# Performance work log

Measured on AMD Instinct MI355X. Metric: run time of the kernel, lower is better.

## Reference

```python
import jax, jax.numpy as jnp
import numpy as np

N = 100_000      # num nodes
R = 7            # num relations
D = 64           # input_dim == output_dim
E = 1_600_000    # num edges
EDIM = 16        # edge_input_dim


def setup_inputs() -> dict:
    key = jax.random.key(0)
    ks = jax.random.split(key, 10)
    node_in = jax.random.randint(ks[0], (E,), 0, N)
    node_out = jax.random.randint(ks[1], (E,), 0, N)
    relation = jax.random.randint(ks[2], (E,), 0, R)
    edge_list = jnp.stack([node_in, node_out, relation], axis=1)  # (E, 3)
    x = jax.random.normal(ks[3], (N, D), dtype=jnp.float32)
    edge_weight = jax.random.uniform(ks[4], (E,), dtype=jnp.float32)
    edge_feature = jax.random.normal(ks[5], (E, EDIM), dtype=jnp.float32)
    s = 1.0 / np.sqrt(R * D)
    W_lin = jax.random.uniform(ks[6], (D, R * D), minval=-s, maxval=s, dtype=jnp.float32)
    b_lin = jnp.zeros((D,), jnp.float32)
    s2 = 1.0 / np.sqrt(D)
    W_self = jax.random.uniform(ks[7], (D, D), minval=-s2, maxval=s2, dtype=jnp.float32)
    b_self = jnp.zeros((D,), jnp.float32)
    s3 = 1.0 / np.sqrt(EDIM)
    W_edge = jax.random.uniform(ks[8], (D, EDIM), minval=-s3, maxval=s3, dtype=jnp.float32)
    b_edge = jnp.zeros((D,), jnp.float32)
    return {"x": x, "edge_list": edge_list, "edge_weight": edge_weight,
            "edge_feature": edge_feature, "W_lin": W_lin, "b_lin": b_lin,
            "W_self": W_self, "b_self": b_self, "W_edge": W_edge, "b_edge": b_edge}


def reference(x, edge_list, edge_weight, edge_feature, W_lin, b_lin, W_self, b_self, W_edge, b_edge):
    node_in, node_out, relation = edge_list[:, 0], edge_list[:, 1], edge_list[:, 2]
    # destination index in the flattened (node, relation) space
    seg = node_out * R + relation  # (E,)
    # sparse.mm(adj.T, x): scatter w * x[src] into (N*R, D)
    msg = edge_weight[:, None] * x[node_in]  # (E, D)
    update = jax.ops.segment_sum(msg, seg, num_segments=N * R)  # (N*R, D)
    # edge feature branch: edge_linear then weighted scatter_add
    edge_msg = (edge_feature @ W_edge.T + b_edge) * edge_weight[:, None]  # (E, D)
    update = update + jax.ops.segment_sum(edge_msg, seg, num_segments=N * R)
    update = update.reshape(N, R * D)
    out = update @ W_lin.T + b_lin + x @ W_self.T + b_self
    return jax.nn.relu(out)
```

## Files before the change

kernel.cpp:

```cpp
#include <hip/hip_runtime.h>
#include <hip/hip_bf16.h>
#include <hip/hip_fp16.h>

#define N_NODES 100000
#define R_REL   7
#define E_EDGES 1600000
#define EDIM    16
#define KTOT    640
#define AROWB   1280
#define CAP     56
#define CSTR    16
#define CHUNK   16


#define ASWZ(row, cb) ((row) * AROWB + ((cb) ^ (((row) & 7) << 4)))

typedef __bf16 bf16_t;
typedef bf16_t bf16x8 __attribute__((ext_vector_type(8)));
typedef float  f32x4  __attribute__((ext_vector_type(4)));
typedef unsigned long long u64;

#define RFL(v) __builtin_amdgcn_readfirstlane(v)
#define RL(v, l) __builtin_amdgcn_readlane(v, l)


__global__ __launch_bounds__(256) void k_pre(
    const float* __restrict__ x, const int* __restrict__ el,
    const float* __restrict__ wgt,
    const float* __restrict__ W_lin, const float* __restrict__ W_self,
    const float* __restrict__ W_edge, const float* __restrict__ b_edge,
    int* __restrict__ cnt, bf16_t* __restrict__ xb, bf16_t* __restrict__ Bp,
    u64* __restrict__ recs8)
{
    const int t = blockIdx.x * 256 + threadIdx.x;

    if (t < (N_NODES * 64) / 16) {
        const float4* xp = (const float4*)(x + (size_t)t * 16);
        float4 v0 = xp[0], v1 = xp[1], v2 = xp[2], v3 = xp[3];
        bf16x8 o0 = {(bf16_t)v0.x, (bf16_t)v0.y, (bf16_t)v0.z, (bf16_t)v0.w,
                     (bf16_t)v1.x, (bf16_t)v1.y, (bf16_t)v1.z, (bf16_t)v1.w};
        bf16x8 o1 = {(bf16_t)v2.x, (bf16_t)v2.y, (bf16_t)v2.z, (bf16_t)v2.w,
                     (bf16_t)v3.x, (bf16_t)v3.y, (bf16_t)v3.z, (bf16_t)v3.w};
        *(bf16x8*)(xb + (size_t)t * 16)     = o0;
        *(bf16x8*)(xb + (size_t)t * 16 + 8) = o1;
    }

    if (t < KTOT * 64) {
        int k = t >> 6;
        int j = t & 63;
        float v;
        if (k < 448) {
            v = W_lin[j * 448 + k];
        } else if (k < 512) {
            v = W_self[j * 64 + (k - 448)];
        } else if (k < 624) {
            int r = (k - 512) >> 4, kk = (k - 512) & 15;
            float sacc = 0.f;
            for (int d = 0; d < 64; d++)
                sacc = fmaf(W_lin[j * 448 + r * 64 + d], W_edge[d * 16 + kk], sacc);
            v = sacc;
        } else if (k < 631) {
            int r = k - 624;
            float sacc = 0.f;
            for (int d = 0; d < 64; d++)
                sacc = fmaf(W_lin[j * 448 + r * 64 + d], b_edge[d], sacc);
            v = sacc;
        } else {
            v = 0.f;
        }
        Bp[((k >> 3) * 64 + j) * 8 + (k & 7)] = (bf16_t)v;
    }

    if (t < E_EDGES / 4) {
        const int4* ep = (const int4*)(el + (size_t)t * 12);
        int4 q0 = ep[0], q1 = ep[1], q2 = ep[2];
        float4 w4 = *(const float4*)(wgt + (size_t)t * 4);
        const int e = t * 4;
        const int srcs[4] = {q0.x, q0.w, q1.z, q2.y};
        const int dsts[4] = {q0.y, q1.x, q1.w, q2.z};
        const int rels[4] = {q0.z, q1.y, q2.x, q2.w};
        const float ws[4] = {w4.x, w4.y, w4.z, w4.w};
        int slot[4];
#pragma unroll
        for (int i = 0; i < 4; i++)
            slot[i] = atomicAdd(&cnt[dsts[i] * CSTR], 1);
#pragma unroll
        for (int i = 0; i < 4; i++) {
            unsigned u0 = (unsigned)srcs[i] | ((unsigned)rels[i] << 17)
                        | ((unsigned)((e + i) & 0xFFF) << 20);
            unsigned u1 = ((unsigned)(e + i) >> 12)
                        | (__float_as_uint(ws[i]) & 0xFFFFFE00u);
            if (slot[i] < CAP)
                recs8[(size_t)slot[i] * N_NODES + dsts[i]] = ((u64)u1 << 32) | u0;
        }
    }
}


__global__ __launch_bounds__(256, 6) void k_main(
    const bf16_t* __restrict__ xb, const float* __restrict__ ef,
    const float* __restrict__ b_lin, const float* __restrict__ b_self,
    const int* __restrict__ cnt, const u64* __restrict__ recs8,
    const bf16_t* __restrict__ Bp, float* __restrict__ out)
{
    __shared__ __align__(16) unsigned char A[16 * AROWB];
    const int wave = threadIdx.x >> 6;
    const int lane = threadIdx.x & 63;
    const int lef  = lane & 15;
    const int nodeBase = blockIdx.x * 16;
    const int n0 = nodeBase + wave * 4;

    int md[4];
    u64 rw[4];
#pragma unroll
    for (int i = 0; i < 4; i++) {
        const int row = wave * 4 + i;
        md[i] = RFL(min(cnt[(n0 + i) * CSTR], CAP));
        rw[i] = (lane < md[i]) ? recs8[(size_t)lane * N_NODES + (n0 + i)] : 0ull;
        *(bf16_t*)(A + ASWZ(row, (448 + lane) * 2)) = xb[(n0 + i) * 64 + lane];
        uint4 z = {0u, 0u, 0u, 0u};
        if (lane < 56) *(uint4*)(A + ASWZ(row, lane * 16)) = z;
        if (lane < 16) *(uint4*)(A + ASWZ(row, 1024 + lane * 16)) = z;
    }

#pragma unroll
    for (int i = 0; i < 4; i++) {
        const int row = wave * 4 + i;
        const int m = md[i];
        if (m == 0) continue;
        const int u0v = (int)(unsigned)rw[i];
        const int u1v = (int)(unsigned)(rw[i] >> 32);
        const int relv = ((unsigned)u0v >> 17) & 7;
        const bool valid = lane < m;

        u64 g0 = __ballot(valid && relv == 0);
        u64 g1 = __ballot(valid && relv == 1);
        u64 g2 = __ballot(valid && relv == 2);
        u64 g3 = __ballot(valid && relv == 3);
        u64 g4 = __ballot(valid && relv == 4);
        u64 g5 = __ballot(valid && relv == 5);
        u64 g6 = __ballot(valid && relv == 6);
        const int c0 = __builtin_popcountll(g0), c1 = __builtin_popcountll(g1);
        const int c2 = __builtin_popcountll(g2), c3 = __builtin_popcountll(g3);
        const int c4 = __builtin_popcountll(g4), c5 = __builtin_popcountll(g5);
        const int p0 = 0, p1 = c0, p2 = p1 + c1, p3 = p2 + c2;
        const int p4 = p3 + c3, p5 = p4 + c4, p6 = p5 + c5;
        const bool b0 = relv & 1, b1 = relv & 2, b2 = relv & 4;
        u64 t0 = b0 ? g1 : g0, t1 = b0 ? g3 : g2, t2 = b0 ? g5 : g4, t3 = g6;
        u64 sA = b1 ? t1 : t0, sB = b1 ? t3 : t2;
        u64 mm = b2 ? sB : sA;
        int pa = b0 ? p1 : p0, pb = b0 ? p3 : p2, pc = b0 ? p5 : p4, pd = p6;
        int pe_ = b1 ? pb : pa, pf_ = b1 ? pd : pc;
        int pfx = b2 ? pf_ : pe_;
        int rig = __builtin_amdgcn_mbcnt_hi((unsigned)(mm >> 32),
                  __builtin_amdgcn_mbcnt_lo((unsigned)mm, 0));
        int rank = valid ? (pfx + rig) : lane;
        const int pv0 = valid ? u0v : (7 << 17);
        const int pv1 = valid ? u1v : 0;
        const int su0 = __builtin_amdgcn_ds_permute(rank * 4, pv0);
        const int su1 = __builtin_amdgcn_ds_permute(rank * 4, pv1);

        float a = 0.f, F = 0.f, sw_ = 0.f;
        int cur = -1;
        for (int base = 0; base < m; base += CHUNK) {
            unsigned short xv[CHUNK];
            float ev[CHUNK], wk[CHUNK];
            int rk[CHUNK];
#pragma unroll
            for (int k = 0; k < CHUNK; k++) {
                const int uu0 = RL(su0, base + k);
                const int uu1 = RL(su1, base + k);
                const int src = uu0 & 0x1FFFF;
                const int e   = (int)(((unsigned)uu0) >> 20)
                              | ((uu1 & 0x1FF) << 12);
                rk[k] = (int)((((unsigned)uu0) >> 17) & 7);
                wk[k] = __uint_as_float((unsigned)uu1 & 0xFFFFFE00u);
                xv[k] = *(const unsigned short*)(xb + ((size_t)src << 6) + lane);
                ev[k] = ef[(size_t)e * EDIM + lef];
            }
#pragma unroll
            for (int k = 0; k < CHUNK; k++) {
                if (rk[k] != cur && rk[k] != 7) {
                    if (cur >= 0) {
                        *(bf16_t*)(A + ASWZ(row, (cur * 64 + lane) * 2)) = (bf16_t)a;
                        if (lane < EDIM)
                            *(bf16_t*)(A + ASWZ(row, (512 + cur * EDIM + lane) * 2)) = (bf16_t)F;
                        if (lane == 0)
                            *(bf16_t*)(A + ASWZ(row, (624 + cur) * 2)) = (bf16_t)sw_;
                    }
                    a = 0.f; F = 0.f; sw_ = 0.f; cur = rk[k];
                }
                const float xf = __uint_as_float(((unsigned)xv[k]) << 16);
                a   = fmaf(wk[k], xf,    a);
                F   = fmaf(wk[k], ev[k], F);
                sw_ += wk[k];
            }
        }
        *(bf16_t*)(A + ASWZ(row, (cur * 64 + lane) * 2)) = (bf16_t)a;
        if (lane < EDIM)
            *(bf16_t*)(A + ASWZ(row, (512 + cur * EDIM + lane) * 2)) = (bf16_t)F;
        if (lane == 0)
            *(bf16_t*)(A + ASWZ(row, (624 + cur) * 2)) = (bf16_t)sw_;
    }
    __syncthreads();

    const int quad = lane >> 4;
    const int l15  = lane & 15;
    const unsigned abase = (unsigned)l15 * AROWB;
    const unsigned aswz  = (unsigned)((l15 & 7) << 4);
    f32x4 c = {0.f, 0.f, 0.f, 0.f};
#pragma unroll
    for (int s2i = 0; s2i < KTOT / 32; s2i++) {
        bf16x8 av = *(const bf16x8*)(A + abase
                     + (((unsigned)(s2i * 64 + quad * 16)) ^ aswz));
        bf16x8 bv = *(const bf16x8*)(Bp + (((s2i * 4 + quad) * 64) + wave * 16 + l15) * 8);
        c = __builtin_amdgcn_mfma_f32_16x16x32_bf16(av, bv, c, 0, 0, 0);
    }
    const int j = wave * 16 + l15;
    const float bias = b_lin[j] + b_self[j];
#pragma unroll
    for (int q = 0; q < 4; q++) {
        const int n = nodeBase + quad * 4 + q;
        float v = c[q] + bias;
        out[n * 64 + j] = v > 0.f ? v : 0.f;
    }
}


extern "C" void kernel_launch(void* const* d_in, const int* in_sizes, int n_in,
                              void* d_out, int out_size, void* d_ws, size_t ws_size,
                              hipStream_t stream) {
    const float* x      = (const float*)d_in[0];
    const int*   el     = (const int*)  d_in[1];
    const float* wgt    = (const float*)d_in[2];
    const float* ef     = (const float*)d_in[3];
    const float* W_lin  = (const float*)d_in[4];
    const float* b_lin  = (const float*)d_in[5];
    const float* W_self = (const float*)d_in[6];
    const float* b_self = (const float*)d_in[7];
    const float* W_edge = (const float*)d_in[8];
    const float* b_edge = (const float*)d_in[9];
    float* out = (float*)d_out;

    u64*    recs8 = (u64*)d_ws;
    int*    cnt   = (int*)(recs8 + (size_t)N_NODES * CAP);
    bf16_t* xb    = (bf16_t*)(cnt + (size_t)N_NODES * CSTR);
    bf16_t* Bp    = xb + (size_t)N_NODES * 64;

    hipMemsetAsync(cnt, 0, (size_t)N_NODES * CSTR * sizeof(int), stream);
    k_pre <<<1563, 256, 0, stream>>>(x, el, wgt, W_lin, W_self, W_edge, b_edge,
                                     cnt, xb, Bp, recs8);
    k_main<<<N_NODES / 16, 256, 0, stream>>>(xb, ef, b_lin, b_self,
                                             cnt, recs8, Bp, out);
}
```

Measured before the change: 371.9 us.

## Partition edge bucketing by destination range to localize atomics and record writes

The edge-bucketing phase now has each block handle one destination partition of 12500 nodes over a slice of the edges. It reads every edge's destination and only processes edges whose destination falls in its partition. The aim is to confine counter atomics and record scatter writes to a smaller address range, improving cache locality on the atomic/scatter traffic. In exchange, every edge's destination is read eight times, and the grid grows to 2048 blocks, which changes how the prologue work (x conversion, B packing) is indexed by thread.

```diff
diff --git a/kernel.cpp b/kernel.cpp
--- a/kernel.cpp
+++ b/kernel.cpp
@@ -11,6 +11,10 @@
 #define CAP     56
 #define CSTR    16
 #define CHUNK   16
+#define NPART   8
+#define NPP     12500
+#define BPP     256
+#define EPB     (E_EDGES / BPP)
 
 
 #define ASWZ(row, cb) ((row) * AROWB + ((cb) ^ (((row) & 7) << 4)))
@@ -71,27 +75,24 @@
         Bp[((k >> 3) * 64 + j) * 8 + (k & 7)] = (bf16_t)v;
     }
 
-    if (t < E_EDGES / 4) {
-        const int4* ep = (const int4*)(el + (size_t)t * 12);
-        int4 q0 = ep[0], q1 = ep[1], q2 = ep[2];
-        float4 w4 = *(const float4*)(wgt + (size_t)t * 4);
-        const int e = t * 4;
-        const int srcs[4] = {q0.x, q0.w, q1.z, q2.y};
-        const int dsts[4] = {q0.y, q1.x, q1.w, q2.z};
-        const int rels[4] = {q0.z, q1.y, q2.x, q2.w};
-        const float ws[4] = {w4.x, w4.y, w4.z, w4.w};
-        int slot[4];
-#pragma unroll
-        for (int i = 0; i < 4; i++)
-            slot[i] = atomicAdd(&cnt[dsts[i] * CSTR], 1);
-#pragma unroll
-        for (int i = 0; i < 4; i++) {
-            unsigned u0 = (unsigned)srcs[i] | ((unsigned)rels[i] << 17)
-                        | ((unsigned)((e + i) & 0xFFF) << 20);
-            unsigned u1 = ((unsigned)(e + i) >> 12)
-                        | (__float_as_uint(ws[i]) & 0xFFFFFE00u);
-            if (slot[i] < CAP)
-                recs8[(size_t)slot[i] * N_NODES + dsts[i]] = ((u64)u1 << 32) | u0;
+    {
+        const int part   = blockIdx.x & (NPART - 1);
+        const int pbase  = part * NPP;
+        const int estart = (blockIdx.x >> 3) * EPB;
+        for (int e = estart + threadIdx.x; e < estart + EPB; e += 256) {
+            const int dst = el[e * 3 + 1];
+            if ((unsigned)(dst - pbase) < (unsigned)NPP) {
+                const int src = el[e * 3];
+                const int rel = el[e * 3 + 2];
+                const float w = wgt[e];
+                const int slot = atomicAdd(&cnt[dst * CSTR], 1);
+                unsigned u0 = (unsigned)src | ((unsigned)rel << 17)
+                            | ((unsigned)(e & 0xFFF) << 20);
+                unsigned u1 = ((unsigned)e >> 12)
+                            | (__float_as_uint(w) & 0xFFFFFE00u);
+                if (slot < CAP)
+                    recs8[(size_t)slot * N_NODES + dst] = ((u64)u1 << 32) | u0;
+            }
         }
     }
 }
@@ -248,8 +249,8 @@
     bf16_t* Bp    = xb + (size_t)N_NODES * 64;
 
     hipMemsetAsync(cnt, 0, (size_t)N_NODES * CSTR * sizeof(int), stream);
-    k_pre <<<1563, 256, 0, stream>>>(x, el, wgt, W_lin, W_self, W_edge, b_edge,
-                                     cnt, xb, Bp, recs8);
+    k_pre <<<NPART * BPP, 256, 0, stream>>>(x, el, wgt, W_lin, W_self, W_edge,
+                                            b_edge, cnt, xb, Bp, recs8);
     k_main<<<N_NODES / 16, 256, 0, stream>>>(xb, ef, b_lin, b_self,
                                              cnt, recs8, Bp, out);
 }
```

Measured after the change: 375.9 us. Within noise of the previous version (+1.1%).
